# Kernel optimization log

Measured on AMD Instinct MI355X. Metric: run time of the kernel, lower is better.

## Reference

```python
import jax, jax.numpy as jnp
import numpy as np

H, KVH, D = 32, 8, 64  # n_heads, n_kv_heads, head_dim
NREP = H // KVH


def _rope(x, cos, sin):
    # x: (B,T,h,D); cos/sin: (T, D//2)
    half = x.shape[-1] // 2
    x1, x2 = x[..., :half], x[..., half:]
    c = cos[None, :, None, :]
    s = sin[None, :, None, :]
    return jnp.concatenate([x1 * c - x2 * s, x1 * s + x2 * c], axis=-1).astype(x.dtype)


def setup_inputs() -> dict:
    key = jax.random.key(0)
    k1, k2, k3 = jax.random.split(key, 3)
    B, T, C = 1, 2048, 2048
    x = jax.random.normal(k1, (B, T, C), dtype=jnp.float32)
    # real RoPE tables (base 10000), shape (T, D//2)
    inv_freq = 1.0 / (10000.0 ** (np.arange(0, D, 2, dtype=np.float32) / D))
    t = np.arange(T, dtype=np.float32)
    freqs = np.outer(t, inv_freq)
    cos = jnp.asarray(np.cos(freqs))
    sin = jnp.asarray(np.sin(freqs))
    Wqkv = jax.random.normal(k2, (C, H * D + 2 * KVH * D), dtype=jnp.float32) * (C ** -0.5)
    Wo = jax.random.normal(k3, (H * D, C), dtype=jnp.float32) * ((H * D) ** -0.5)
    return {"x": x, "cos": cos, "sin": sin, "Wqkv": Wqkv, "Wo": Wo}


def reference(x, cos, sin, Wqkv, Wo):
    B, T, C = x.shape
    qkv = x @ Wqkv  # (B,T, H*D + 2*KVH*D)
    q = qkv[..., : H * D].reshape(B, T, H, D)
    k = qkv[..., H * D : H * D + KVH * D].reshape(B, T, KVH, D)
    v = qkv[..., H * D + KVH * D :].reshape(B, T, KVH, D)
    # cast to bf16 as in the torch module
    q, k, v = q.astype(jnp.bfloat16), k.astype(jnp.bfloat16), v.astype(jnp.bfloat16)
    q = _rope(q, cos, sin)
    k = _rope(k, cos, sin)
    # GQA without materializing repeated KV: split q heads into (kv_head, rep)
    qg = q.reshape(B, T, KVH, NREP, D)
    scale = jnp.asarray(1.0 / np.sqrt(D), dtype=jnp.bfloat16)
    scores = jnp.einsum("bqhrd,bkhd->bhrqk", qg, k) * scale  # (B,KVH,NREP,T,T) bf16
    causal = jnp.tril(jnp.ones((T, T), dtype=bool))
    scores = jnp.where(causal[None, None, None], scores, jnp.asarray(-jnp.inf, scores.dtype))
    attn = jax.nn.softmax(scores.astype(jnp.float32), axis=-1).astype(q.dtype)
    out = jnp.einsum("bhrqk,bkhd->bqhrd", attn, v).reshape(B, T, H * D)
    return out.astype(jnp.float32) @ Wo
```

## Files before the change

### kernel.cpp

```cpp
#include <hip/hip_runtime.h>
#include <hip/hip_bf16.h>
#include <cstdint>
#include <cstddef>

#define T_SEQ 2048
#define C_DIM 2048
#define NQKV  3072
#define HQ    32
#define KVH_  8
#define D_HEAD 64

using bf16x8 = __attribute__((ext_vector_type(8))) __bf16;
using f32x4  = __attribute__((ext_vector_type(4))) float;

typedef const __attribute__((address_space(1))) void* gas_ptr;
typedef __attribute__((address_space(3))) void* las_ptr;
#define GLOAD_LDS16(g, l) __builtin_amdgcn_global_load_lds((gas_ptr)(g), (las_ptr)(l), 16, 0, 0)

static __device__ __forceinline__ unsigned short f2bf(float f) {
  union { float f; unsigned int u; } v; v.f = f;
  unsigned int u = v.u;
  unsigned int r = u + 0x7fffu + ((u >> 16) & 1u);
  return (unsigned short)(r >> 16);
}
static __device__ __forceinline__ float bf2f(unsigned short s) {
  union { unsigned int u; float f; } v; v.u = ((unsigned int)s) << 16;
  return v.f;
}
static __device__ __forceinline__ bf16x8 load8(const unsigned short* p) {
  return *reinterpret_cast<const bf16x8*>(p);
}
static __device__ __forceinline__ f32x4 mfma16(bf16x8 a, bf16x8 b, f32x4 c) {
  return __builtin_amdgcn_mfma_f32_16x16x32_bf16(a, b, c, 0, 0, 0);
}

static __device__ const unsigned char kF2QG[40] = {
    15, 15, 15, 15, 14, 14, 14, 13, 13, 13, 12, 12, 12, 11, 11,
    10, 10, 9, 9, 8, 8, 7, 7, 6, 5, 4, 3,
    14, 11, 6, 2, 13, 10, 5, 1, 12, 9, 8, 4, 0};
static __device__ const unsigned char kF2SEG[40] = {
    0, 1, 2, 3, 0, 1, 2, 0, 1, 2, 0, 1, 2, 0, 1,
    0, 1, 0, 1, 0, 1, 0, 1, 0, 0, 0, 0,
    3, 2, 1, 0, 3, 2, 1, 0, 3, 2, 2, 1, 0};
static __device__ const unsigned char kQGF[16][4] = {
    {39, 0, 0, 0}, {34, 0, 0, 0}, {30, 0, 0, 0}, {26, 0, 0, 0},
    {25, 38, 0, 0}, {24, 33, 0, 0}, {23, 29, 0, 0}, {21, 22, 0, 0},
    {19, 20, 37, 0}, {17, 18, 36, 0}, {15, 16, 32, 0}, {13, 14, 28, 0},
    {10, 11, 12, 35}, {7, 8, 9, 31}, {4, 5, 6, 27}, {0, 1, 2, 3}};

__global__ __launch_bounds__(256) void cast_x_kernel(
    const float* __restrict__ x, unsigned short* __restrict__ xh) {
  const int i = (blockIdx.x * 256 + threadIdx.x) * 8;
  const float4 a = *reinterpret_cast<const float4*>(x + i);
  const float4 b = *reinterpret_cast<const float4*>(x + i + 4);
  ushort h[8];
  h[0] = f2bf(a.x); h[1] = f2bf(a.y); h[2] = f2bf(a.z); h[3] = f2bf(a.w);
  h[4] = f2bf(b.x); h[5] = f2bf(b.y); h[6] = f2bf(b.z); h[7] = f2bf(b.w);
  *reinterpret_cast<uint4*>(xh + i) = *reinterpret_cast<const uint4*>(h);
}

__global__ __launch_bounds__(256) void transpose_cast_kernel(
    const float* __restrict__ src, unsigned short* __restrict__ dhi, int R, int C) {
  __shared__ float tile[64][65];
  const int r0 = blockIdx.y * 64, c0 = blockIdx.x * 64;
  const int tid = threadIdx.x;
  const int lr = tid >> 4, lc = (tid & 15) * 4;
  for (int i = 0; i < 4; ++i) {
    const int row = lr + i * 16;
    const float4 v = *reinterpret_cast<const float4*>(&src[(size_t)(r0 + row) * C + c0 + lc]);
    tile[row][lc + 0] = v.x; tile[row][lc + 1] = v.y;
    tile[row][lc + 2] = v.z; tile[row][lc + 3] = v.w;
  }
  __syncthreads();
  for (int i = 0; i < 4; ++i) {
    const int n = lr + i * 16;
    ushort4 h;
    h.x = f2bf(tile[lc + 0][n]); h.y = f2bf(tile[lc + 1][n]);
    h.z = f2bf(tile[lc + 2][n]); h.w = f2bf(tile[lc + 3][n]);
    *reinterpret_cast<ushort4*>(&dhi[(size_t)(c0 + n) * R + r0 + lc]) = h;
  }
}

__global__ __launch_bounds__(256, 2) void gemm1_kernel(
    const unsigned short* __restrict__ Xh, const unsigned short* __restrict__ BTh,
    const float* __restrict__ cosb, const float* __restrict__ sinb,
    unsigned short* __restrict__ qkv) {
  __shared__ unsigned short Ah[64 * 64], Bh[128 * 64];
  const int tid = threadIdx.x;
  const int orig = (int)blockIdx.y * 24 + (int)blockIdx.x;
  const int wgid = (orig & 7) * 96 + (orig >> 3);
  const int n0 = (wgid % 24) * 128, m0 = (wgid / 24) * 64;
  const int lane = tid & 63, wave = tid >> 6;
  const int wm = wave >> 1, wn = wave & 1;
  const int lrow = lane & 15, g = lane >> 4;
  const int srow8 = lane >> 3, pchunk = lane & 7;
  const int swz = lrow & 7;
  f32x4 acc[2][4] = {};
  for (int kb = 0; kb < C_DIM; kb += 64) {
    __syncthreads();
    for (int p = 0; p < 2; ++p) {
      const int row = (p * 4 + wave) * 8 + srow8;
      const int gcol = (pchunk ^ srow8) * 8;
      GLOAD_LDS16(&Xh[(size_t)(m0 + row) * C_DIM + kb + gcol],
                  &Ah[row * 64 + pchunk * 8]);
    }
    for (int p = 0; p < 4; ++p) {
      const int row = (p * 4 + wave) * 8 + srow8;
      const int gcol = (pchunk ^ srow8) * 8;
      GLOAD_LDS16(&BTh[(size_t)(n0 + row) * C_DIM + kb + gcol],
                  &Bh[row * 64 + pchunk * 8]);
    }
    __syncthreads();
    for (int kk = 0; kk < 2; ++kk) {
      bf16x8 ah[2], bh[4];
      const int cc = ((kk * 4 + g) ^ swz) * 8;
      for (int i = 0; i < 2; ++i)
        ah[i] = load8(&Ah[(wm * 32 + i * 16 + lrow) * 64 + cc]);
      for (int i = 0; i < 4; ++i)
        bh[i] = load8(&Bh[(wn * 64 + i * 16 + lrow) * 64 + cc]);
      for (int mi = 0; mi < 2; ++mi)
        for (int ni = 0; ni < 4; ++ni)
          acc[mi][ni] = mfma16(ah[mi], bh[ni], acc[mi][ni]);
    }
  }
  const int colbase = n0 + wn * 64;
  const bool isv = colbase >= (C_DIM + KVH_ * D_HEAD);
  const float qsc = (colbase < C_DIM) ? 0.125f : 1.0f;
  for (int mi = 0; mi < 2; ++mi) {
    for (int r = 0; r < 4; ++r) {
      const int trow = m0 + wm * 32 + mi * 16 + g * 4 + r;
      if (!isv) {
        for (int ni = 0; ni < 2; ++ni) {
          const int dh = ni * 16 + lrow;
          const float c = cosb[trow * 32 + dh];
          const float s = sinb[trow * 32 + dh];
          const float a = bf2f(f2bf(acc[mi][ni][r]));
          const float b = bf2f(f2bf(acc[mi][ni + 2][r]));
          qkv[(size_t)trow * NQKV + colbase + dh]      = f2bf((a * c - b * s) * qsc);
          qkv[(size_t)trow * NQKV + colbase + dh + 32] = f2bf((a * s + b * c) * qsc);
        }
      } else {
        for (int ni = 0; ni < 4; ++ni)
          qkv[(size_t)trow * NQKV + colbase + ni * 16 + lrow] = f2bf(acc[mi][ni][r]);
      }
    }
  }
}

__global__ __launch_bounds__(256) void vt_kernel(const unsigned short* __restrict__ qkv,
                                                 unsigned short* __restrict__ vt) {
  __shared__ unsigned short tile[64][72];
  const int t0 = blockIdx.x * 64, j0 = blockIdx.y * 64;
  const int tid = threadIdx.x;
  const int lr = tid >> 4, lc = (tid & 15) * 4;
  for (int i = 0; i < 4; ++i) {
    const int row = lr + i * 16;
    const ushort4 v = *reinterpret_cast<const ushort4*>(
        &qkv[(size_t)(t0 + row) * NQKV + (C_DIM + KVH_ * D_HEAD) + j0 + lc]);
    *reinterpret_cast<ushort4*>(&tile[row][lc]) = v;
  }
  __syncthreads();
  for (int i = 0; i < 4; ++i) {
    const int j = lr + i * 16;
    ushort4 v;
    v.x = tile[lc + 0][j]; v.y = tile[lc + 1][j];
    v.z = tile[lc + 2][j]; v.w = tile[lc + 3][j];
    *reinterpret_cast<ushort4*>(&vt[(size_t)(j0 + j) * T_SEQ + t0 + lc]) = v;
  }
}

__global__ __launch_bounds__(256, 3) void attn_seg_kernel(
    const unsigned short* __restrict__ qkv, const unsigned short* __restrict__ Vt,
    unsigned short* __restrict__ po, float2* __restrict__ pml) {
  __shared__ unsigned short kbuf[2][64 * 64];
  __shared__ unsigned short vbuf[2][64 * 64];
  __shared__ unsigned short plds[4][2][16][72];
  const int f = blockIdx.x, h = blockIdx.y;
  const int qg = kF2QG[f];
  const int seg = kF2SEG[f];
  const int slot = h * 40 + f;
  const int tid = threadIdx.x;
  const int wave = tid >> 6, lane = tid & 63;
  const int kvh = h >> 2;
  const int q0b = qg * 128;
  const int q0 = q0b + wave * 32;
  const int lrow = lane & 15, g = lane >> 4;

  const int t0 = seg * 8;
  const int t1 = min(t0 + 8, 2 * qg + 2);

  const int srow = lane >> 3;
  const int schunk = (lane & 7) ^ srow;
  const unsigned short* Kg = qkv + C_DIM + kvh * D_HEAD;

  bf16x8 qf[2][2];
  for (int qs = 0; qs < 2; ++qs)
    for (int dc = 0; dc < 2; ++dc)
      qf[qs][dc] = load8(&qkv[(size_t)(q0 + qs * 16 + lrow) * NQKV + h * D_HEAD + dc * 32 + g * 8]);

  f32x4 o[2][4] = {};
  float l_[2] = {0.f, 0.f};
  const int swz = (lrow & 7);

  {
    const int k00 = t0 * 64;
    for (int j = 0; j < 2; ++j) {
      const int r0 = wave * 16 + j * 8;
      GLOAD_LDS16(Kg + (size_t)(k00 + r0 + srow) * NQKV + schunk * 8,
                  &kbuf[0][r0 * 64 + lane * 8]);
      GLOAD_LDS16(Vt + (size_t)(kvh * 64 + r0 + srow) * T_SEQ + k00 + schunk * 8,
                  &vbuf[0][r0 * 64 + lane * 8]);
    }
  }
  __syncthreads();

  for (int t = t0; t < t1; ++t) {
    const int cur = (t - t0) & 1;
    const int k0 = t * 64;
    if (t + 1 < t1) {
      const int k0n = k0 + 64;
      for (int j = 0; j < 2; ++j) {
        const int r0 = wave * 16 + j * 8;
        GLOAD_LDS16(Kg + (size_t)(k0n + r0 + srow) * NQKV + schunk * 8,
                    &kbuf[cur ^ 1][r0 * 64 + lane * 8]);
        GLOAD_LDS16(Vt + (size_t)(kvh * 64 + r0 + srow) * T_SEQ + k0n + schunk * 8,
                    &vbuf[cur ^ 1][r0 * 64 + lane * 8]);
      }
    }

    if (k0 <= q0 + 31) {
      const bool maskt = (k0 + 63 > q0);

      f32x4 s[4][2] = {};
      __builtin_amdgcn_s_setprio(1);
      for (int kt = 0; kt < 4; ++kt) {
        const unsigned short* krow = &kbuf[cur][(kt * 16 + lrow) * 64];
        const bf16x8 kf0 = load8(krow + ((0 * 4 + g) ^ swz) * 8);
        const bf16x8 kf1 = load8(krow + ((1 * 4 + g) ^ swz) * 8);
        for (int qs = 0; qs < 2; ++qs) {
          s[kt][qs] = mfma16(kf0, qf[qs][0], s[kt][qs]);
          s[kt][qs] = mfma16(kf1, qf[qs][1], s[kt][qs]);
        }
      }
      __builtin_amdgcn_s_setprio(0);

      for (int qs = 0; qs < 2; ++qs) {
        float rs = 0.f;
        for (int kt = 0; kt < 4; ++kt)
          for (int r = 0; r < 4; ++r) {
            float v = (float)(__bf16)(s[kt][qs][r]);
            if (maskt) {
              const int ka = k0 + kt * 16 + 4 * g + r;
              const int qa = q0 + qs * 16 + lrow;
              v = (ka <= qa) ? v : -INFINITY;
            }
            const float p = __expf(v);
            s[kt][qs][r] = p;
            rs += p;
          }
        l_[qs] += rs;
      }

      for (int qs = 0; qs < 2; ++qs)
        for (int kt = 0; kt < 4; ++kt) {
          union { __bf16 h4[4]; unsigned long long u; } w;
          for (int r = 0; r < 4; ++r) w.h4[r] = (__bf16)(s[kt][qs][r]);
          *reinterpret_cast<unsigned long long*>(
              &plds[wave][qs][lrow][kt * 16 + 4 * g]) = w.u;
        }
      asm volatile("s_waitcnt lgkmcnt(0)" ::: "memory");

      __builtin_amdgcn_s_setprio(1);
      for (int kc = 0; kc < 2; ++kc) {
        const bf16x8 pf0 = load8(&plds[wave][0][lrow][kc * 32 + g * 8]);
        const bf16x8 pf1 = load8(&plds[wave][1][lrow][kc * 32 + g * 8]);
        for (int dt = 0; dt < 4; ++dt) {
          const bf16x8 vf =
              load8(&vbuf[cur][(dt * 16 + lrow) * 64 + ((kc * 4 + g) ^ swz) * 8]);
          o[0][dt] = mfma16(vf, pf0, o[0][dt]);
          o[1][dt] = mfma16(vf, pf1, o[1][dt]);
        }
      }
      __builtin_amdgcn_s_setprio(0);
    }
    __syncthreads();
  }

  for (int qs = 0; qs < 2; ++qs) {
    float lv = l_[qs];
    lv += __shfl_xor(lv, 16);
    lv += __shfl_xor(lv, 32);
    l_[qs] = lv;
  }
  unsigned short* ol = &plds[wave][0][0][0];
  for (int qs = 0; qs < 2; ++qs) {
    const float inv = 1.f / l_[qs];
    for (int dt = 0; dt < 4; ++dt) {
      union { __bf16 h4[4]; unsigned long long u; } w;
      for (int r = 0; r < 4; ++r) w.h4[r] = (__bf16)(o[qs][dt][r] * inv);
      *reinterpret_cast<unsigned long long*>(
          &ol[(qs * 16 + lrow) * 72 + dt * 16 + 4 * g]) = w.u;
    }
  }
  asm volatile("s_waitcnt lgkmcnt(0)" ::: "memory");
  for (int rr = 0; rr < 4; ++rr) {
    const int row = rr * 8 + (lane >> 3);
    const int cs = (lane & 7) * 8;
    const bf16x8 v = load8(&ol[row * 72 + cs]);
    *reinterpret_cast<bf16x8*>(
        &po[(size_t)slot * 8192 + (wave * 32 + row) * 64 + cs]) = v;
  }
  if (g == 0)
    for (int qs = 0; qs < 2; ++qs)
      pml[slot * 128 + wave * 32 + qs * 16 + lrow] = make_float2(0.f, l_[qs]);
}

__global__ __launch_bounds__(256) void attn_combine_kernel(
    const unsigned short* __restrict__ po, const float2* __restrict__ pml,
    unsigned short* __restrict__ aout) {
  const int qg = blockIdx.x, h = blockIdx.y;
  const int nseg = (2 * qg + 9) / 8;
  const int tid = threadIdx.x;
  const int row = tid >> 1, c0 = (tid & 1) * 32;
  float L = 0.f, w[4];
  for (int s = 0; s < nseg; ++s) {
    const int slot = h * 40 + kQGF[qg][s];
    w[s] = pml[slot * 128 + row].y;
    L += w[s];
  }
  float acc[32] = {};
  for (int s = 0; s < nseg; ++s) {
    const int slot = h * 40 + kQGF[qg][s];
    const unsigned short* p = &po[(size_t)slot * 8192 + row * 64 + c0];
    for (int j = 0; j < 4; ++j) {
      const bf16x8 v = load8(p + j * 8);
      for (int e = 0; e < 8; ++e) acc[j * 8 + e] += w[s] * (float)v[e];
    }
  }
  const float invL = 1.f / L;
  for (int j = 0; j < 4; ++j) {
    __bf16 ov[8];
    for (int e = 0; e < 8; ++e) ov[e] = (__bf16)(acc[j * 8 + e] * invL);
    *reinterpret_cast<bf16x8*>(
        &aout[(size_t)(qg * 128 + row) * C_DIM + h * D_HEAD + c0 + j * 8]) =
        *reinterpret_cast<const bf16x8*>(ov);
  }
}

__global__ __launch_bounds__(256, 2) void gemm3_kernel(
    const unsigned short* __restrict__ A, const unsigned short* __restrict__ BT,
    float* __restrict__ out) {
  __shared__ unsigned short As[64 * 64], Bs[128 * 64];
  const int tid = threadIdx.x;
  const int orig = (int)blockIdx.y * 16 + (int)blockIdx.x;
  const int wgid = (orig & 7) * 64 + (orig >> 3);
  const int n0 = (wgid % 16) * 128, m0 = (wgid / 16) * 64;
  const int lane = tid & 63, wave = tid >> 6;
  const int wm = wave >> 1, wn = wave & 1;
  const int lrow = lane & 15, g = lane >> 4;
  const int srow8 = lane >> 3, pchunk = lane & 7;
  const int swz = lrow & 7;
  f32x4 acc[2][4] = {};
  for (int kb = 0; kb < C_DIM; kb += 64) {
    __syncthreads();
    for (int p = 0; p < 2; ++p) {
      const int row = (p * 4 + wave) * 8 + srow8;
      const int gcol = (pchunk ^ srow8) * 8;
      GLOAD_LDS16(&A[(size_t)(m0 + row) * C_DIM + kb + gcol],
                  &As[row * 64 + pchunk * 8]);
    }
    for (int p = 0; p < 4; ++p) {
      const int row = (p * 4 + wave) * 8 + srow8;
      const int gcol = (pchunk ^ srow8) * 8;
      GLOAD_LDS16(&BT[(size_t)(n0 + row) * C_DIM + kb + gcol],
                  &Bs[row * 64 + pchunk * 8]);
    }
    __syncthreads();
    for (int kk = 0; kk < 2; ++kk) {
      bf16x8 af[2], bfr[4];
      const int cc = ((kk * 4 + g) ^ swz) * 8;
      for (int i = 0; i < 2; ++i)
        af[i] = load8(&As[(wm * 32 + i * 16 + lrow) * 64 + cc]);
      for (int i = 0; i < 4; ++i)
        bfr[i] = load8(&Bs[(wn * 64 + i * 16 + lrow) * 64 + cc]);
      for (int mi = 0; mi < 2; ++mi)
        for (int ni = 0; ni < 4; ++ni)
          acc[mi][ni] = mfma16(af[mi], bfr[ni], acc[mi][ni]);
    }
  }
  for (int mi = 0; mi < 2; ++mi)
    for (int ni = 0; ni < 4; ++ni)
      for (int r = 0; r < 4; ++r)
        out[(size_t)(m0 + wm * 32 + mi * 16 + g * 4 + r) * C_DIM +
            n0 + wn * 64 + ni * 16 + lrow] = acc[mi][ni][r];
}

extern "C" void kernel_launch(void* const* d_in, const int* in_sizes, int n_in,
                              void* d_out, int out_size, void* d_ws, size_t ws_size,
                              hipStream_t stream) {
  (void)in_sizes; (void)n_in; (void)out_size; (void)ws_size;
  const float* x    = (const float*)d_in[0];
  const float* cosb = (const float*)d_in[1];
  const float* sinb = (const float*)d_in[2];
  const float* Wqkv = (const float*)d_in[3];
  const float* Wo   = (const float*)d_in[4];
  float* out = (float*)d_out;

  unsigned short* WqkvT_hi = (unsigned short*)d_ws;
  unsigned short* WoT      = WqkvT_hi + (size_t)NQKV * C_DIM;
  unsigned short* qkv      = WoT + (size_t)C_DIM * C_DIM;
  unsigned short* Vt       = qkv + (size_t)T_SEQ * NQKV;
  unsigned short* aout     = Vt + (size_t)KVH_ * D_HEAD * T_SEQ;
  unsigned short* Xh       = aout + (size_t)T_SEQ * C_DIM;
  unsigned short* po  = Xh;
  float2*         pml = (float2*)d_ws;

  cast_x_kernel<<<(T_SEQ * C_DIM) / (256 * 8), 256, 0, stream>>>(x, Xh);
  transpose_cast_kernel<<<dim3(NQKV / 64, C_DIM / 64), 256, 0, stream>>>(
      Wqkv, WqkvT_hi, C_DIM, NQKV);
  transpose_cast_kernel<<<dim3(C_DIM / 64, C_DIM / 64), 256, 0, stream>>>(
      Wo, WoT, C_DIM, C_DIM);
  gemm1_kernel<<<dim3(24, 32), 256, 0, stream>>>(Xh, WqkvT_hi, cosb, sinb, qkv);
  vt_kernel<<<dim3(T_SEQ / 64, (KVH_ * D_HEAD) / 64), 256, 0, stream>>>(qkv, Vt);
  attn_seg_kernel<<<dim3(40, HQ), 256, 0, stream>>>(qkv, Vt, po, pml);
  attn_combine_kernel<<<dim3(16, HQ), 256, 0, stream>>>(po, pml, aout);
  gemm3_kernel<<<dim3(16, 32), 256, 0, stream>>>(aout, WoT, out);
}
```

Measured before the change: 134.9 us.

## Use 512-thread attention blocks covering 256 queries to halve K/V tile loads

The attention segment kernel now runs 8 waves per block covering 256 query rows instead of 128, so each K/V tile staged in shared memory is reused by twice as many queries. Each wave issues one async load instead of two, and the grid shrinks to 20 work items per head with new segment tables. Partial outputs are also stored unnormalized, so the combine kernel just sums them and divides by the total sum. This cuts global K/V traffic and per-block overhead, but leaves fewer blocks to balance, makes causal-edge waves sit idle longer, and writes unnormalized partials to bf16.

Result: slower. 139.9 us (+3.8%).

```diff
diff --git a/kernel.cpp b/kernel.cpp
--- a/kernel.cpp
+++ b/kernel.cpp
@@ -34,19 +34,13 @@
   return __builtin_amdgcn_mfma_f32_16x16x32_bf16(a, b, c, 0, 0, 0);
 }
 
-static __device__ const unsigned char kF2QG[40] = {
-    15, 15, 15, 15, 14, 14, 14, 13, 13, 13, 12, 12, 12, 11, 11,
-    10, 10, 9, 9, 8, 8, 7, 7, 6, 5, 4, 3,
-    14, 11, 6, 2, 13, 10, 5, 1, 12, 9, 8, 4, 0};
-static __device__ const unsigned char kF2SEG[40] = {
-    0, 1, 2, 3, 0, 1, 2, 0, 1, 2, 0, 1, 2, 0, 1,
-    0, 1, 0, 1, 0, 1, 0, 1, 0, 0, 0, 0,
-    3, 2, 1, 0, 3, 2, 1, 0, 3, 2, 2, 1, 0};
-static __device__ const unsigned char kQGF[16][4] = {
-    {39, 0, 0, 0}, {34, 0, 0, 0}, {30, 0, 0, 0}, {26, 0, 0, 0},
-    {25, 38, 0, 0}, {24, 33, 0, 0}, {23, 29, 0, 0}, {21, 22, 0, 0},
-    {19, 20, 37, 0}, {17, 18, 36, 0}, {15, 16, 32, 0}, {13, 14, 28, 0},
-    {10, 11, 12, 35}, {7, 8, 9, 31}, {4, 5, 6, 27}, {0, 1, 2, 3}};
+static __device__ const unsigned char kF2B[20] = {
+    7, 7, 7, 7, 6, 6, 6, 5, 5, 5, 4, 4, 3, 3, 2, 1, 6, 4, 2, 0};
+static __device__ const unsigned char kF2SEG[20] = {
+    0, 1, 2, 3, 0, 1, 2, 0, 1, 2, 0, 1, 0, 1, 0, 0, 3, 2, 1, 0};
+static __device__ const unsigned char kBQGF[8][4] = {
+    {19, 0, 0, 0}, {15, 0, 0, 0}, {14, 18, 0, 0}, {12, 13, 0, 0},
+    {10, 11, 17, 0}, {7, 8, 9, 0}, {4, 5, 6, 16}, {0, 1, 2, 3}};
 
 __global__ __launch_bounds__(256) void cast_x_kernel(
     const float* __restrict__ x, unsigned short* __restrict__ xh) {
@@ -169,25 +163,24 @@
   }
 }
 
-__global__ __launch_bounds__(256, 3) void attn_seg_kernel(
+__global__ __launch_bounds__(512, 2) void attn_seg_kernel(
     const unsigned short* __restrict__ qkv, const unsigned short* __restrict__ Vt,
     unsigned short* __restrict__ po, float2* __restrict__ pml) {
   __shared__ unsigned short kbuf[2][64 * 64];
   __shared__ unsigned short vbuf[2][64 * 64];
-  __shared__ unsigned short plds[4][2][16][72];
+  __shared__ unsigned short plds[8][2][16][72];
   const int f = blockIdx.x, h = blockIdx.y;
-  const int qg = kF2QG[f];
+  const int b = kF2B[f];
   const int seg = kF2SEG[f];
-  const int slot = h * 40 + f;
+  const int slot = h * 20 + f;
   const int tid = threadIdx.x;
   const int wave = tid >> 6, lane = tid & 63;
   const int kvh = h >> 2;
-  const int q0b = qg * 128;
-  const int q0 = q0b + wave * 32;
+  const int q0 = b * 256 + wave * 32;
   const int lrow = lane & 15, g = lane >> 4;
 
   const int t0 = seg * 8;
-  const int t1 = min(t0 + 8, 2 * qg + 2);
+  const int t1 = min(t0 + 8, 4 * b + 4);
 
   const int srow = lane >> 3;
   const int schunk = (lane & 7) ^ srow;
@@ -204,13 +197,11 @@
 
   {
     const int k00 = t0 * 64;
-    for (int j = 0; j < 2; ++j) {
-      const int r0 = wave * 16 + j * 8;
-      GLOAD_LDS16(Kg + (size_t)(k00 + r0 + srow) * NQKV + schunk * 8,
-                  &kbuf[0][r0 * 64 + lane * 8]);
-      GLOAD_LDS16(Vt + (size_t)(kvh * 64 + r0 + srow) * T_SEQ + k00 + schunk * 8,
-                  &vbuf[0][r0 * 64 + lane * 8]);
-    }
+    const int r0 = wave * 8;
+    GLOAD_LDS16(Kg + (size_t)(k00 + r0 + srow) * NQKV + schunk * 8,
+                &kbuf[0][r0 * 64 + lane * 8]);
+    GLOAD_LDS16(Vt + (size_t)(kvh * 64 + r0 + srow) * T_SEQ + k00 + schunk * 8,
+                &vbuf[0][r0 * 64 + lane * 8]);
   }
   __syncthreads();
 
@@ -219,13 +210,11 @@
     const int k0 = t * 64;
     if (t + 1 < t1) {
       const int k0n = k0 + 64;
-      for (int j = 0; j < 2; ++j) {
-        const int r0 = wave * 16 + j * 8;
-        GLOAD_LDS16(Kg + (size_t)(k0n + r0 + srow) * NQKV + schunk * 8,
-                    &kbuf[cur ^ 1][r0 * 64 + lane * 8]);
-        GLOAD_LDS16(Vt + (size_t)(kvh * 64 + r0 + srow) * T_SEQ + k0n + schunk * 8,
-                    &vbuf[cur ^ 1][r0 * 64 + lane * 8]);
-      }
+      const int r0 = wave * 8;
+      GLOAD_LDS16(Kg + (size_t)(k0n + r0 + srow) * NQKV + schunk * 8,
+                  &kbuf[cur ^ 1][r0 * 64 + lane * 8]);
+      GLOAD_LDS16(Vt + (size_t)(kvh * 64 + r0 + srow) * T_SEQ + k0n + schunk * 8,
+                  &vbuf[cur ^ 1][r0 * 64 + lane * 8]);
     }
 
     if (k0 <= q0 + 31) {
@@ -294,10 +283,9 @@
   }
   unsigned short* ol = &plds[wave][0][0][0];
   for (int qs = 0; qs < 2; ++qs) {
-    const float inv = 1.f / l_[qs];
     for (int dt = 0; dt < 4; ++dt) {
       union { __bf16 h4[4]; unsigned long long u; } w;
-      for (int r = 0; r < 4; ++r) w.h4[r] = (__bf16)(o[qs][dt][r] * inv);
+      for (int r = 0; r < 4; ++r) w.h4[r] = (__bf16)(o[qs][dt][r]);
       *reinterpret_cast<unsigned long long*>(
           &ol[(qs * 16 + lrow) * 72 + dt * 16 + 4 * g]) = w.u;
     }
@@ -308,33 +296,34 @@
     const int cs = (lane & 7) * 8;
     const bf16x8 v = load8(&ol[row * 72 + cs]);
     *reinterpret_cast<bf16x8*>(
-        &po[(size_t)slot * 8192 + (wave * 32 + row) * 64 + cs]) = v;
+        &po[(size_t)slot * 16384 + (wave * 32 + row) * 64 + cs]) = v;
   }
   if (g == 0)
     for (int qs = 0; qs < 2; ++qs)
-      pml[slot * 128 + wave * 32 + qs * 16 + lrow] = make_float2(0.f, l_[qs]);
+      pml[slot * 256 + wave * 32 + qs * 16 + lrow] = make_float2(0.f, l_[qs]);
 }
 
 __global__ __launch_bounds__(256) void attn_combine_kernel(
     const unsigned short* __restrict__ po, const float2* __restrict__ pml,
     unsigned short* __restrict__ aout) {
   const int qg = blockIdx.x, h = blockIdx.y;
+  const int b = qg >> 1, half = qg & 1;
   const int nseg = (2 * qg + 9) / 8;
   const int tid = threadIdx.x;
   const int row = tid >> 1, c0 = (tid & 1) * 32;
-  float L = 0.f, w[4];
+  float L = 0.f;
   for (int s = 0; s < nseg; ++s) {
-    const int slot = h * 40 + kQGF[qg][s];
-    w[s] = pml[slot * 128 + row].y;
-    L += w[s];
+    const int slot = h * 20 + kBQGF[b][s];
+    L += pml[slot * 256 + half * 128 + row].y;
   }
   float acc[32] = {};
   for (int s = 0; s < nseg; ++s) {
-    const int slot = h * 40 + kQGF[qg][s];
-    const unsigned short* p = &po[(size_t)slot * 8192 + row * 64 + c0];
+    const int slot = h * 20 + kBQGF[b][s];
+    const unsigned short* p =
+        &po[(size_t)slot * 16384 + (half * 128 + row) * 64 + c0];
     for (int j = 0; j < 4; ++j) {
       const bf16x8 v = load8(p + j * 8);
-      for (int e = 0; e < 8; ++e) acc[j * 8 + e] += w[s] * (float)v[e];
+      for (int e = 0; e < 8; ++e) acc[j * 8 + e] += (float)v[e];
     }
   }
   const float invL = 1.f / L;
@@ -422,7 +411,7 @@
       Wo, WoT, C_DIM, C_DIM);
   gemm1_kernel<<<dim3(24, 32), 256, 0, stream>>>(Xh, WqkvT_hi, cosb, sinb, qkv);
   vt_kernel<<<dim3(T_SEQ / 64, (KVH_ * D_HEAD) / 64), 256, 0, stream>>>(qkv, Vt);
-  attn_seg_kernel<<<dim3(40, HQ), 256, 0, stream>>>(qkv, Vt, po, pml);
+  attn_seg_kernel<<<dim3(20, HQ), 512, 0, stream>>>(qkv, Vt, po, pml);
   attn_combine_kernel<<<dim3(16, HQ), 256, 0, stream>>>(po, pml, aout);
   gemm3_kernel<<<dim3(16, 32), 256, 0, stream>>>(aout, WoT, out);
 }
```

## Double-buffer LDS tiles in QKV and output-projection GEMMs to overlap loads

Applied to the files above, without the earlier changes.

Both GEMM kernels now keep two LDS buffers for the A and B tiles. The next K-slice is prefetched with global_load_lds into the alternate buffer while MFMAs run on the current one, and one barrier per iteration replaces two. The goal is to hide global-memory latency behind compute. In exchange, LDS use per block doubles to 48KB, which may limit occupancy. The single barrier also relies on the async loads being complete when __syncthreads is reached, since the compiler inserts vmcnt waits.

After: 137.9 us. 1.02x slower.

```diff
diff --git a/kernel.cpp b/kernel.cpp
--- a/kernel.cpp
+++ b/kernel.cpp
@@ -85,7 +85,7 @@
     const unsigned short* __restrict__ Xh, const unsigned short* __restrict__ BTh,
     const float* __restrict__ cosb, const float* __restrict__ sinb,
     unsigned short* __restrict__ qkv) {
-  __shared__ unsigned short Ah[64 * 64], Bh[128 * 64];
+  __shared__ unsigned short Ah[2][64 * 64], Bh[2][128 * 64];
   const int tid = threadIdx.x;
   const int orig = (int)blockIdx.y * 24 + (int)blockIdx.x;
   const int wgid = (orig & 7) * 96 + (orig >> 3);
@@ -95,34 +95,48 @@
   const int lrow = lane & 15, g = lane >> 4;
   const int srow8 = lane >> 3, pchunk = lane & 7;
   const int swz = lrow & 7;
+  const int gcolS = (pchunk ^ srow8) * 8;
+
+  for (int p = 0; p < 2; ++p) {
+    const int row = (p * 4 + wave) * 8 + srow8;
+    GLOAD_LDS16(&Xh[(size_t)(m0 + row) * C_DIM + gcolS], &Ah[0][row * 64 + pchunk * 8]);
+  }
+  for (int p = 0; p < 4; ++p) {
+    const int row = (p * 4 + wave) * 8 + srow8;
+    GLOAD_LDS16(&BTh[(size_t)(n0 + row) * C_DIM + gcolS], &Bh[0][row * 64 + pchunk * 8]);
+  }
+  __syncthreads();
+
   f32x4 acc[2][4] = {};
-  for (int kb = 0; kb < C_DIM; kb += 64) {
-    __syncthreads();
-    for (int p = 0; p < 2; ++p) {
-      const int row = (p * 4 + wave) * 8 + srow8;
-      const int gcol = (pchunk ^ srow8) * 8;
-      GLOAD_LDS16(&Xh[(size_t)(m0 + row) * C_DIM + kb + gcol],
-                  &Ah[row * 64 + pchunk * 8]);
-    }
-    for (int p = 0; p < 4; ++p) {
-      const int row = (p * 4 + wave) * 8 + srow8;
-      const int gcol = (pchunk ^ srow8) * 8;
-      GLOAD_LDS16(&BTh[(size_t)(n0 + row) * C_DIM + kb + gcol],
-                  &Bh[row * 64 + pchunk * 8]);
-    }
-    __syncthreads();
+  for (int t = 0; t < C_DIM / 64; ++t) {
+    const int cur = t & 1;
+    if (t + 1 < C_DIM / 64) {
+      const int kb = (t + 1) * 64;
+      for (int p = 0; p < 2; ++p) {
+        const int row = (p * 4 + wave) * 8 + srow8;
+        GLOAD_LDS16(&Xh[(size_t)(m0 + row) * C_DIM + kb + gcolS],
+                    &Ah[cur ^ 1][row * 64 + pchunk * 8]);
+      }
+      for (int p = 0; p < 4; ++p) {
+        const int row = (p * 4 + wave) * 8 + srow8;
+        GLOAD_LDS16(&BTh[(size_t)(n0 + row) * C_DIM + kb + gcolS],
+                    &Bh[cur ^ 1][row * 64 + pchunk * 8]);
+      }
+    }
     for (int kk = 0; kk < 2; ++kk) {
       bf16x8 ah[2], bh[4];
       const int cc = ((kk * 4 + g) ^ swz) * 8;
       for (int i = 0; i < 2; ++i)
-        ah[i] = load8(&Ah[(wm * 32 + i * 16 + lrow) * 64 + cc]);
+        ah[i] = load8(&Ah[cur][(wm * 32 + i * 16 + lrow) * 64 + cc]);
       for (int i = 0; i < 4; ++i)
-        bh[i] = load8(&Bh[(wn * 64 + i * 16 + lrow) * 64 + cc]);
+        bh[i] = load8(&Bh[cur][(wn * 64 + i * 16 + lrow) * 64 + cc]);
       for (int mi = 0; mi < 2; ++mi)
         for (int ni = 0; ni < 4; ++ni)
           acc[mi][ni] = mfma16(ah[mi], bh[ni], acc[mi][ni]);
     }
-  }
+    __syncthreads();
+  }
+
   const int colbase = n0 + wn * 64;
   const bool isv = colbase >= (C_DIM + KVH_ * D_HEAD);
   const float qsc = (colbase < C_DIM) ? 0.125f : 1.0f;
@@ -350,7 +364,7 @@
 __global__ __launch_bounds__(256, 2) void gemm3_kernel(
     const unsigned short* __restrict__ A, const unsigned short* __restrict__ BT,
     float* __restrict__ out) {
-  __shared__ unsigned short As[64 * 64], Bs[128 * 64];
+  __shared__ unsigned short As[2][64 * 64], Bs[2][128 * 64];
   const int tid = threadIdx.x;
   const int orig = (int)blockIdx.y * 16 + (int)blockIdx.x;
   const int wgid = (orig & 7) * 64 + (orig >> 3);
@@ -360,33 +374,46 @@
   const int lrow = lane & 15, g = lane >> 4;
   const int srow8 = lane >> 3, pchunk = lane & 7;
   const int swz = lrow & 7;
+  const int gcolS = (pchunk ^ srow8) * 8;
+
+  for (int p = 0; p < 2; ++p) {
+    const int row = (p * 4 + wave) * 8 + srow8;
+    GLOAD_LDS16(&A[(size_t)(m0 + row) * C_DIM + gcolS], &As[0][row * 64 + pchunk * 8]);
+  }
+  for (int p = 0; p < 4; ++p) {
+    const int row = (p * 4 + wave) * 8 + srow8;
+    GLOAD_LDS16(&BT[(size_t)(n0 + row) * C_DIM + gcolS], &Bs[0][row * 64 + pchunk * 8]);
+  }
+  __syncthreads();
+
   f32x4 acc[2][4] = {};
-  for (int kb = 0; kb < C_DIM; kb += 64) {
-    __syncthreads();
-    for (int p = 0; p < 2; ++p) {
-      const int row = (p * 4 + wave) * 8 + srow8;
-      const int gcol = (pchunk ^ srow8) * 8;
-      GLOAD_LDS16(&A[(size_t)(m0 + row) * C_DIM + kb + gcol],
-                  &As[row * 64 + pchunk * 8]);
-    }
-    for (int p = 0; p < 4; ++p) {
-      const int row = (p * 4 + wave) * 8 + srow8;
-      const int gcol = (pchunk ^ srow8) * 8;
-      GLOAD_LDS16(&BT[(size_t)(n0 + row) * C_DIM + kb + gcol],
-                  &Bs[row * 64 + pchunk * 8]);
-    }
-    __syncthreads();
+  for (int t = 0; t < C_DIM / 64; ++t) {
+    const int cur = t & 1;
+    if (t + 1 < C_DIM / 64) {
+      const int kb = (t + 1) * 64;
+      for (int p = 0; p < 2; ++p) {
+        const int row = (p * 4 + wave) * 8 + srow8;
+        GLOAD_LDS16(&A[(size_t)(m0 + row) * C_DIM + kb + gcolS],
+                    &As[cur ^ 1][row * 64 + pchunk * 8]);
+      }
+      for (int p = 0; p < 4; ++p) {
+        const int row = (p * 4 + wave) * 8 + srow8;
+        GLOAD_LDS16(&BT[(size_t)(n0 + row) * C_DIM + kb + gcolS],
+                    &Bs[cur ^ 1][row * 64 + pchunk * 8]);
+      }
+    }
     for (int kk = 0; kk < 2; ++kk) {
       bf16x8 af[2], bfr[4];
       const int cc = ((kk * 4 + g) ^ swz) * 8;
       for (int i = 0; i < 2; ++i)
-        af[i] = load8(&As[(wm * 32 + i * 16 + lrow) * 64 + cc]);
+        af[i] = load8(&As[cur][(wm * 32 + i * 16 + lrow) * 64 + cc]);
       for (int i = 0; i < 4; ++i)
-        bfr[i] = load8(&Bs[(wn * 64 + i * 16 + lrow) * 64 + cc]);
+        bfr[i] = load8(&Bs[cur][(wn * 64 + i * 16 + lrow) * 64 + cc]);
       for (int mi = 0; mi < 2; ++mi)
         for (int ni = 0; ni < 4; ++ni)
           acc[mi][ni] = mfma16(af[mi], bfr[ni], acc[mi][ni]);
     }
+    __syncthreads();
   }
   for (int mi = 0; mi < 2; ++mi)
     for (int ni = 0; ni < 4; ++ni)
```
